# Kernel optimization log

Hardware: AMD Instinct MI355X
Metric: run time of the kernel (lower is better)

## Reference

```python
import jax, jax.numpy as jnp
import numpy as np

N = 16_777_216  # total samples in batch
S = 1024        # number of distinct stations/basins
EPS = 1e-6


def setup_inputs() -> dict:
    key = jax.random.key(0)
    k1, k2, k3, k4 = jax.random.split(key, 4)
    y_pred = jax.random.normal(k1, (N,), dtype=jnp.float32)
    y_true = jax.random.normal(k2, (N,), dtype=jnp.float32)
    stations = jax.random.randint(k3, (N,), 0, S, dtype=jnp.int32)
    # per-station observed-discharge std (kept away from 0 for realism)
    station_std = jax.random.uniform(k4, (S,), dtype=jnp.float32) + 0.5
    return {"y_pred": y_pred, "y_true": y_true, "stations": stations,
            "station_std": station_std}


def reference(y_pred, y_true, stations, station_std):
    y_pred = y_pred.reshape(-1)
    y_true = y_true.reshape(-1)
    err2 = (y_pred - y_true) ** 2                                   # [N]
    sse = jax.ops.segment_sum(err2, stations, num_segments=S)       # [S]
    cnt = jax.ops.segment_sum(jnp.ones_like(err2), stations, num_segments=S)
    mse = sse / jnp.maximum(cnt, 1.0)                                # per-station MSE
    denom = (station_std + EPS) ** 2                                 # (sigma+eps)^2
    present = cnt > 0                                                # stations in batch
    per_station = jnp.where(present, mse / denom, 0.0)
    n_present = jnp.maximum(jnp.sum(present.astype(jnp.float32)), 1.0)
    return jnp.sum(per_station) / n_present
```

## Files before the change

kernel.cpp:

```cpp
#include <hip/hip_runtime.h>

#define NUM_S 1024
#define NCOPY 4
constexpr float EPS = 1e-6f;

constexpr int CNT_SHIFT = 44;
constexpr unsigned long long SSE_MASK = (1ULL << 44) - 1;
constexpr double FP_INV_SCALE = 1.0 / 1048576.0;

constexpr int U32_CNT_SHIFT = 24;
constexpr unsigned U32_SSE_MASK = (1u << 24) - 1;
constexpr float FP_SCALE_U32 = 4096.0f;

#define MAX_PBLOCKS 512
#define RED_BLOCKS 32

__global__ __launch_bounds__(1024, 2) void nse_partial_kernel(
    const float4* __restrict__ yp4, const float4* __restrict__ yt4,
    const int4* __restrict__ st4, const float* __restrict__ yp,
    const float* __restrict__ yt, const int* __restrict__ st,
    unsigned long long* __restrict__ g_part,
    unsigned int* __restrict__ g_ctl, int n, int n4)
{
    __shared__ unsigned s_hist[NCOPY * NUM_S];
    for (int i = threadIdx.x; i < NCOPY * NUM_S; i += blockDim.x) {
        s_hist[i] = 0u;
    }
    if (blockIdx.x == 0 && threadIdx.x == 0) {
        g_ctl[0] = 0u;
        ((float*)g_ctl)[1] = 0.0f;
        ((float*)g_ctl)[2] = 0.0f;
    }
    __syncthreads();

    unsigned* hist = s_hist + ((threadIdx.x >> 6) & (NCOPY - 1)) * NUM_S;

    const int gtid = blockIdx.x * blockDim.x + threadIdx.x;
    const int stride = gridDim.x * blockDim.x;
    const unsigned ONE_CNT = 1u << U32_CNT_SHIFT;

    for (int i = gtid; i < n4; i += stride) {
        float4 p = yp4[i];
        float4 t = yt4[i];
        int4 s = st4[i];
        float dx = p.x - t.x;
        float dy = p.y - t.y;
        float dz = p.z - t.z;
        float dw = p.w - t.w;
        unsigned fx = (unsigned)(dx * dx * FP_SCALE_U32 + 0.5f);
        unsigned fy = (unsigned)(dy * dy * FP_SCALE_U32 + 0.5f);
        unsigned fz = (unsigned)(dz * dz * FP_SCALE_U32 + 0.5f);
        unsigned fw = (unsigned)(dw * dw * FP_SCALE_U32 + 0.5f);
        atomicAdd(&hist[s.x], ONE_CNT | fx);
        atomicAdd(&hist[s.y], ONE_CNT | fy);
        atomicAdd(&hist[s.z], ONE_CNT | fz);
        atomicAdd(&hist[s.w], ONE_CNT | fw);
    }
    for (int i = n4 * 4 + gtid; i < n; i += stride) {
        float d = yp[i] - yt[i];
        unsigned f = (unsigned)(d * d * FP_SCALE_U32 + 0.5f);
        atomicAdd(&hist[st[i]], ONE_CNT | f);
    }
    __syncthreads();

    unsigned long long* dst = g_part + (size_t)blockIdx.x * NUM_S;
    for (int i = threadIdx.x; i < NUM_S; i += blockDim.x) {
        unsigned long long h = 0ULL;
        #pragma unroll
        for (int c = 0; c < NCOPY; ++c) {
            unsigned v = s_hist[i + c * NUM_S];
            h += ((unsigned long long)(v >> U32_CNT_SHIFT) << CNT_SHIFT) |
                 ((unsigned long long)(v & U32_SSE_MASK) << 8);
        }
        dst[i] = h;
    }
}

__global__ __launch_bounds__(1024) void nse_reduce_kernel(
    const unsigned long long* __restrict__ g_part,
    const float* __restrict__ station_std,
    unsigned int* __restrict__ g_ctl,
    float* __restrict__ out, int nblocks)
{
    __shared__ unsigned long long s_part[1024];
    const int t = threadIdx.x;
    const int s_lo = blockIdx.x * 32;
    const int ss = s_lo + (t & 31);
    const int chunk = t >> 5;
    const int per_chunk = (nblocks + 31) >> 5;
    const int b0 = chunk * per_chunk;
    const int b1 = min(b0 + per_chunk, nblocks);

    unsigned long long acc = 0ULL;
    for (int b = b0; b < b1; ++b) {
        acc += g_part[(size_t)b * NUM_S + ss];
    }
    s_part[t] = acc;
    __syncthreads();

    float per = 0.0f, pres = 0.0f;
    if (t < 32) {
        unsigned long long h = 0ULL;
        #pragma unroll
        for (int c = 0; c < 32; ++c) {
            h += s_part[t + (c << 5)];
        }
        float cnt = (float)(unsigned)(h >> CNT_SHIFT);
        if (cnt > 0.0f) {
            float sse = (float)((double)(h & SSE_MASK) * FP_INV_SCALE);
            float sd = station_std[s_lo + t];
            float denom = (sd + EPS) * (sd + EPS);
            per = (sse / cnt) / denom;
            pres = 1.0f;
        }
    }

    if (t < 64) {
        #pragma unroll
        for (int o = 32; o > 0; o >>= 1) {
            per += __shfl_down(per, o, 64);
            pres += __shfl_down(pres, o, 64);
        }
        if (t == 0) {
            atomicAdd((float*)g_ctl + 1, per);
            atomicAdd((float*)g_ctl + 2, pres);
            __threadfence();
            unsigned int old = atomicAdd(g_ctl, 1u);
            if (old == gridDim.x - 1) {
                float sp = atomicAdd((float*)g_ctl + 1, 0.0f);
                float sc = atomicAdd((float*)g_ctl + 2, 0.0f);
                out[0] = sp / fmaxf(sc, 1.0f);
            }
        }
    }
}

extern "C" void kernel_launch(void* const* d_in, const int* in_sizes, int n_in,
                              void* d_out, int out_size, void* d_ws, size_t ws_size,
                              hipStream_t stream) {
    const float* y_pred = (const float*)d_in[0];
    const float* y_true = (const float*)d_in[1];
    const int* stations = (const int*)d_in[2];
    const float* station_std = (const float*)d_in[3];
    float* out = (float*)d_out;

    const int n = in_sizes[0];
    const int n4 = n / 4;

    unsigned int* g_ctl = (unsigned int*)d_ws;
    unsigned long long* g_part =
        (unsigned long long*)((char*)d_ws + 64);

    long long avail = ((long long)ws_size - 64) / (NUM_S * 8);
    int npart = (int)(avail < 1 ? 1 : (avail > MAX_PBLOCKS ? MAX_PBLOCKS : avail));

    dim3 grid1(npart);
    dim3 block(1024);
    nse_partial_kernel<<<grid1, block, 0, stream>>>(
        (const float4*)y_pred, (const float4*)y_true, (const int4*)stations,
        y_pred, y_true, stations, g_part, g_ctl, n, n4);

    dim3 grid2(RED_BLOCKS);
    nse_reduce_kernel<<<grid2, block, 0, stream>>>(
        g_part, station_std, g_ctl, out, npart);
}
```

Baseline: 202.7 us.

## Split histogram atomics between LDS and replicated global 64-bit bins

Half of each float4's samples now go to 8 replicated global 64-bit histograms via global atomics, and the other half stay in the shared-memory histograms. The aim is to take pressure off the LDS atomic units by using global/L2 atomics in parallel. The reduce kernel adds the replicas into its sums, and a memset clears them along with the control words. The cost is heavy contention on global atomics, with about 8M global 64-bit atomics across only 8K addresses, plus an extra memset call.

```diff
diff --git a/kernel.cpp b/kernel.cpp
--- a/kernel.cpp
+++ b/kernel.cpp
@@ -2,11 +2,13 @@
 
 #define NUM_S 1024
 #define NCOPY 4
+#define NREP 8
 constexpr float EPS = 1e-6f;
 
 constexpr int CNT_SHIFT = 44;
 constexpr unsigned long long SSE_MASK = (1ULL << 44) - 1;
 constexpr double FP_INV_SCALE = 1.0 / 1048576.0;
+constexpr float FP_SCALE_20 = 1048576.0f;
 
 constexpr int U32_CNT_SHIFT = 24;
 constexpr unsigned U32_SSE_MASK = (1u << 24) - 1;
@@ -20,24 +22,21 @@
     const int4* __restrict__ st4, const float* __restrict__ yp,
     const float* __restrict__ yt, const int* __restrict__ st,
     unsigned long long* __restrict__ g_part,
-    unsigned int* __restrict__ g_ctl, int n, int n4)
+    unsigned long long* __restrict__ g_rep, int n, int n4)
 {
     __shared__ unsigned s_hist[NCOPY * NUM_S];
     for (int i = threadIdx.x; i < NCOPY * NUM_S; i += blockDim.x) {
         s_hist[i] = 0u;
     }
-    if (blockIdx.x == 0 && threadIdx.x == 0) {
-        g_ctl[0] = 0u;
-        ((float*)g_ctl)[1] = 0.0f;
-        ((float*)g_ctl)[2] = 0.0f;
-    }
     __syncthreads();
 
     unsigned* hist = s_hist + ((threadIdx.x >> 6) & (NCOPY - 1)) * NUM_S;
+    unsigned long long* grep = g_rep + (blockIdx.x & (NREP - 1)) * NUM_S;
 
     const int gtid = blockIdx.x * blockDim.x + threadIdx.x;
     const int stride = gridDim.x * blockDim.x;
-    const unsigned ONE_CNT = 1u << U32_CNT_SHIFT;
+    const unsigned ONE_CNT32 = 1u << U32_CNT_SHIFT;
+    const unsigned long long ONE_CNT64 = 1ULL << CNT_SHIFT;
 
     for (int i = gtid; i < n4; i += stride) {
         float4 p = yp4[i];
@@ -49,17 +48,17 @@
         float dw = p.w - t.w;
         unsigned fx = (unsigned)(dx * dx * FP_SCALE_U32 + 0.5f);
         unsigned fy = (unsigned)(dy * dy * FP_SCALE_U32 + 0.5f);
-        unsigned fz = (unsigned)(dz * dz * FP_SCALE_U32 + 0.5f);
-        unsigned fw = (unsigned)(dw * dw * FP_SCALE_U32 + 0.5f);
-        atomicAdd(&hist[s.x], ONE_CNT | fx);
-        atomicAdd(&hist[s.y], ONE_CNT | fy);
-        atomicAdd(&hist[s.z], ONE_CNT | fz);
-        atomicAdd(&hist[s.w], ONE_CNT | fw);
+        atomicAdd(&hist[s.x], ONE_CNT32 | fx);
+        atomicAdd(&hist[s.y], ONE_CNT32 | fy);
+        unsigned fz = (unsigned)(dz * dz * FP_SCALE_20 + 0.5f);
+        unsigned fw = (unsigned)(dw * dw * FP_SCALE_20 + 0.5f);
+        atomicAdd(&grep[s.z], ONE_CNT64 | (unsigned long long)fz);
+        atomicAdd(&grep[s.w], ONE_CNT64 | (unsigned long long)fw);
     }
     for (int i = n4 * 4 + gtid; i < n; i += stride) {
         float d = yp[i] - yt[i];
         unsigned f = (unsigned)(d * d * FP_SCALE_U32 + 0.5f);
-        atomicAdd(&hist[st[i]], ONE_CNT | f);
+        atomicAdd(&hist[st[i]], ONE_CNT32 | f);
     }
     __syncthreads();
 
@@ -78,6 +77,7 @@
 
 __global__ __launch_bounds__(1024) void nse_reduce_kernel(
     const unsigned long long* __restrict__ g_part,
+    const unsigned long long* __restrict__ g_rep,
     const float* __restrict__ station_std,
     unsigned int* __restrict__ g_ctl,
     float* __restrict__ out, int nblocks)
@@ -104,6 +104,10 @@
         #pragma unroll
         for (int c = 0; c < 32; ++c) {
             h += s_part[t + (c << 5)];
+        }
+        #pragma unroll
+        for (int r = 0; r < NREP; ++r) {
+            h += g_rep[r * NUM_S + s_lo + t];
         }
         float cnt = (float)(unsigned)(h >> CNT_SHIFT);
         if (cnt > 0.0f) {
@@ -148,19 +152,24 @@
     const int n4 = n / 4;
 
     unsigned int* g_ctl = (unsigned int*)d_ws;
+    unsigned long long* g_rep =
+        (unsigned long long*)((char*)d_ws + 64);
     unsigned long long* g_part =
-        (unsigned long long*)((char*)d_ws + 64);
+        (unsigned long long*)((char*)d_ws + 64 + NREP * NUM_S * 8);
 
-    long long avail = ((long long)ws_size - 64) / (NUM_S * 8);
+    hipMemsetAsync(d_ws, 0, 64 + NREP * NUM_S * 8, stream);
+
+    long long avail =
+        ((long long)ws_size - 64 - NREP * NUM_S * 8) / (NUM_S * 8);
     int npart = (int)(avail < 1 ? 1 : (avail > MAX_PBLOCKS ? MAX_PBLOCKS : avail));
 
     dim3 grid1(npart);
     dim3 block(1024);
     nse_partial_kernel<<<grid1, block, 0, stream>>>(
         (const float4*)y_pred, (const float4*)y_true, (const int4*)stations,
-        y_pred, y_true, stations, g_part, g_ctl, n, n4);
+        y_pred, y_true, stations, g_part, g_rep, n, n4);
 
     dim3 grid2(RED_BLOCKS);
     nse_reduce_kernel<<<grid2, block, 0, stream>>>(
-        g_part, station_std, g_ctl, out, npart);
+        g_part, g_rep, station_std, g_ctl, out, npart);
 }
```

New measurement: 464.8 us. 129% more time.

## Replace LDS atomics with per-wave private histograms and ballot-based match serialization

Applied to the files above, without the earlier changes.

Gives each wavefront its own private 1024-bin LDS histogram (16 copies instead of 4) and replaces the shared-memory atomicAdd with a match-any style scheme. Ten ballots identify lanes sharing the same station, and those lanes then perform serialized volatile read-modify-writes, one leader per round. The aim is to remove LDS atomic cost and inter-wave contention. In exchange it adds about ten ballots per element plus a loop whose trip count is the largest group of duplicate stations in a wave, and LDS use grows to 64KB per block, which may limit occupancy. The final merge also reads 16 copies per bin.

```diff
diff --git a/kernel.cpp b/kernel.cpp
--- a/kernel.cpp
+++ b/kernel.cpp
@@ -1,7 +1,7 @@
 #include <hip/hip_runtime.h>
 
 #define NUM_S 1024
-#define NCOPY 4
+#define NWAVE 16
 constexpr float EPS = 1e-6f;
 
 constexpr int CNT_SHIFT = 44;
@@ -11,9 +11,34 @@
 constexpr int U32_CNT_SHIFT = 24;
 constexpr unsigned U32_SSE_MASK = (1u << 24) - 1;
 constexpr float FP_SCALE_U32 = 4096.0f;
+constexpr unsigned ONE_CNT32 = 1u << U32_CNT_SHIFT;
 
 #define MAX_PBLOCKS 512
 #define RED_BLOCKS 32
+
+__device__ __forceinline__ void accum_one(unsigned* hist, int s, unsigned val)
+{
+    const int lane = threadIdx.x & 63;
+    unsigned long long peers = ~0ULL;
+    #pragma unroll
+    for (int b = 0; b < 10; ++b) {
+        unsigned long long vote = __ballot((s >> b) & 1);
+        peers &= ((s >> b) & 1) ? vote : ~vote;
+    }
+    bool done = false;
+    for (;;) {
+        unsigned long long rem = __ballot(!done);
+        if (rem == 0ULL) break;
+        if (!done) {
+            int leader = __ffsll(peers & rem) - 1;
+            if (leader == lane) {
+                volatile unsigned* h = hist + s;
+                *h = *h + val;
+                done = true;
+            }
+        }
+    }
+}
 
 __global__ __launch_bounds__(1024, 2) void nse_partial_kernel(
     const float4* __restrict__ yp4, const float4* __restrict__ yt4,
@@ -22,8 +47,8 @@
     unsigned long long* __restrict__ g_part,
     unsigned int* __restrict__ g_ctl, int n, int n4)
 {
-    __shared__ unsigned s_hist[NCOPY * NUM_S];
-    for (int i = threadIdx.x; i < NCOPY * NUM_S; i += blockDim.x) {
+    __shared__ unsigned s_hist[NWAVE * NUM_S];
+    for (int i = threadIdx.x; i < NWAVE * NUM_S; i += blockDim.x) {
         s_hist[i] = 0u;
     }
     if (blockIdx.x == 0 && threadIdx.x == 0) {
@@ -33,11 +58,10 @@
     }
     __syncthreads();
 
-    unsigned* hist = s_hist + ((threadIdx.x >> 6) & (NCOPY - 1)) * NUM_S;
+    unsigned* hist = s_hist + (threadIdx.x >> 6) * NUM_S;
 
     const int gtid = blockIdx.x * blockDim.x + threadIdx.x;
     const int stride = gridDim.x * blockDim.x;
-    const unsigned ONE_CNT = 1u << U32_CNT_SHIFT;
 
     for (int i = gtid; i < n4; i += stride) {
         float4 p = yp4[i];
@@ -51,15 +75,15 @@
         unsigned fy = (unsigned)(dy * dy * FP_SCALE_U32 + 0.5f);
         unsigned fz = (unsigned)(dz * dz * FP_SCALE_U32 + 0.5f);
         unsigned fw = (unsigned)(dw * dw * FP_SCALE_U32 + 0.5f);
-        atomicAdd(&hist[s.x], ONE_CNT | fx);
-        atomicAdd(&hist[s.y], ONE_CNT | fy);
-        atomicAdd(&hist[s.z], ONE_CNT | fz);
-        atomicAdd(&hist[s.w], ONE_CNT | fw);
+        accum_one(hist, s.x, ONE_CNT32 | fx);
+        accum_one(hist, s.y, ONE_CNT32 | fy);
+        accum_one(hist, s.z, ONE_CNT32 | fz);
+        accum_one(hist, s.w, ONE_CNT32 | fw);
     }
     for (int i = n4 * 4 + gtid; i < n; i += stride) {
         float d = yp[i] - yt[i];
         unsigned f = (unsigned)(d * d * FP_SCALE_U32 + 0.5f);
-        atomicAdd(&hist[st[i]], ONE_CNT | f);
+        atomicAdd(&hist[st[i]], ONE_CNT32 | f);
     }
     __syncthreads();
 
@@ -67,7 +91,7 @@
     for (int i = threadIdx.x; i < NUM_S; i += blockDim.x) {
         unsigned long long h = 0ULL;
         #pragma unroll
-        for (int c = 0; c < NCOPY; ++c) {
+        for (int c = 0; c < NWAVE; ++c) {
             unsigned v = s_hist[i + c * NUM_S];
             h += ((unsigned long long)(v >> U32_CNT_SHIFT) << CNT_SHIFT) |
                  ((unsigned long long)(v & U32_SSE_MASK) << 8);
```

Measured after the change: 215.4 us. 6.3% more time.

## Replace LDS atomics with per-wave tagged write-readback histograms

Applied to the files above, without the earlier changes.

Gives each wavefront its own shared-memory histogram and replaces atomicAdd with a software tag-and-retry update: each lane writes its sum tagged with its lane id, then reads the value back to detect collisions with other lanes in the same wave. The goal is to avoid the cost of LDS atomics and contention between waves. In exchange, the packed fields shrink to a 5-bit count and a 21-bit fixed-point SSE at a coarser scale (256), which raises quantization error and overflow risk. The update loop also depends on same-wave write ordering, so correctness hinges on how the hardware resolves conflicting lane writes.

```diff
diff --git a/kernel.cpp b/kernel.cpp
--- a/kernel.cpp
+++ b/kernel.cpp
@@ -1,19 +1,34 @@
 #include <hip/hip_runtime.h>
 
 #define NUM_S 1024
-#define NCOPY 4
+#define NWAVE 16
 constexpr float EPS = 1e-6f;
 
 constexpr int CNT_SHIFT = 44;
 constexpr unsigned long long SSE_MASK = (1ULL << 44) - 1;
 constexpr double FP_INV_SCALE = 1.0 / 1048576.0;
 
-constexpr int U32_CNT_SHIFT = 24;
-constexpr unsigned U32_SSE_MASK = (1u << 24) - 1;
-constexpr float FP_SCALE_U32 = 4096.0f;
+constexpr unsigned DATA_MASK = 0x03FFFFFFu;
+constexpr unsigned SSE21_MASK = 0x001FFFFFu;
+constexpr int CNT21_SHIFT = 21;
+constexpr float FP_SCALE_U32 = 256.0f;
+constexpr unsigned ONE_CNT21 = 1u << CNT21_SHIFT;
 
 #define MAX_PBLOCKS 512
 #define RED_BLOCKS 32
+
+__device__ __forceinline__ void accum_tag(volatile unsigned* hist, int s,
+                                          unsigned val, unsigned mytag)
+{
+    unsigned h = hist[s];
+    for (;;) {
+        unsigned nv = ((h & DATA_MASK) + val) | mytag;
+        hist[s] = nv;
+        unsigned rb = hist[s];
+        if (rb == nv) break;
+        h = rb;
+    }
+}
 
 __global__ __launch_bounds__(1024, 2) void nse_partial_kernel(
     const float4* __restrict__ yp4, const float4* __restrict__ yt4,
@@ -22,8 +37,8 @@
     unsigned long long* __restrict__ g_part,
     unsigned int* __restrict__ g_ctl, int n, int n4)
 {
-    __shared__ unsigned s_hist[NCOPY * NUM_S];
-    for (int i = threadIdx.x; i < NCOPY * NUM_S; i += blockDim.x) {
+    __shared__ unsigned s_hist[NWAVE * NUM_S];
+    for (int i = threadIdx.x; i < NWAVE * NUM_S; i += blockDim.x) {
         s_hist[i] = 0u;
     }
     if (blockIdx.x == 0 && threadIdx.x == 0) {
@@ -33,11 +48,11 @@
     }
     __syncthreads();
 
-    unsigned* hist = s_hist + ((threadIdx.x >> 6) & (NCOPY - 1)) * NUM_S;
+    volatile unsigned* hist = s_hist + (threadIdx.x >> 6) * NUM_S;
+    const unsigned mytag = (threadIdx.x & 63u) << 26;
 
     const int gtid = blockIdx.x * blockDim.x + threadIdx.x;
     const int stride = gridDim.x * blockDim.x;
-    const unsigned ONE_CNT = 1u << U32_CNT_SHIFT;
 
     for (int i = gtid; i < n4; i += stride) {
         float4 p = yp4[i];
@@ -51,15 +66,15 @@
         unsigned fy = (unsigned)(dy * dy * FP_SCALE_U32 + 0.5f);
         unsigned fz = (unsigned)(dz * dz * FP_SCALE_U32 + 0.5f);
         unsigned fw = (unsigned)(dw * dw * FP_SCALE_U32 + 0.5f);
-        atomicAdd(&hist[s.x], ONE_CNT | fx);
-        atomicAdd(&hist[s.y], ONE_CNT | fy);
-        atomicAdd(&hist[s.z], ONE_CNT | fz);
-        atomicAdd(&hist[s.w], ONE_CNT | fw);
+        accum_tag(hist, s.x, ONE_CNT21 | fx, mytag);
+        accum_tag(hist, s.y, ONE_CNT21 | fy, mytag);
+        accum_tag(hist, s.z, ONE_CNT21 | fz, mytag);
+        accum_tag(hist, s.w, ONE_CNT21 | fw, mytag);
     }
     for (int i = n4 * 4 + gtid; i < n; i += stride) {
         float d = yp[i] - yt[i];
         unsigned f = (unsigned)(d * d * FP_SCALE_U32 + 0.5f);
-        atomicAdd(&hist[st[i]], ONE_CNT | f);
+        accum_tag(hist, st[i], ONE_CNT21 | f, mytag);
     }
     __syncthreads();
 
@@ -67,10 +82,10 @@
     for (int i = threadIdx.x; i < NUM_S; i += blockDim.x) {
         unsigned long long h = 0ULL;
         #pragma unroll
-        for (int c = 0; c < NCOPY; ++c) {
-            unsigned v = s_hist[i + c * NUM_S];
-            h += ((unsigned long long)(v >> U32_CNT_SHIFT) << CNT_SHIFT) |
-                 ((unsigned long long)(v & U32_SSE_MASK) << 8);
+        for (int c = 0; c < NWAVE; ++c) {
+            unsigned v = s_hist[i + c * NUM_S] & DATA_MASK;
+            h += ((unsigned long long)(v >> CNT21_SHIFT) << CNT_SHIFT) |
+                 ((unsigned long long)(v & SSE21_MASK) << 12);
         }
         dst[i] = h;
     }
```

Result: no change. 205.7 us (+1.5%).
